# Kernel optimization log

Hardware: AMD Instinct MI355X
Metric: run time of the kernel (lower is better)

## Reference

```python
import jax, jax.numpy as jnp
import numpy as np

WINDOW_SIZE = 11
NUM_BINS = 256
SIGMA = 1.5
C1 = 0.01 ** 2
C2 = 0.03 ** 2
MAX_PSNR = 40.0


def _gaussian_window():
    xs = jnp.arange(WINDOW_SIZE, dtype=jnp.float32)
    g = jnp.exp(-((xs - WINDOW_SIZE // 2) ** 2) / (2.0 * SIGMA ** 2))
    g = g / g.sum()
    w2 = jnp.outer(g, g)  # [11,11]
    return jnp.broadcast_to(w2[None, None], (3, 1, WINDOW_SIZE, WINDOW_SIZE))


def setup_inputs() -> dict:
    key = jax.random.key(0)
    k1, k2 = jax.random.split(key)
    B, C, H, W = 64, 3, 256, 256
    x = jax.random.uniform(k1, (B, C, H, W), dtype=jnp.float32) * 2.0 - 1.0
    y = jax.random.uniform(k2, (B, C, H, W), dtype=jnp.float32) * 2.0 - 1.0
    return {"x": x, "y": y, "window": _gaussian_window()}


def _depthwise_conv(img, w):
    pad = WINDOW_SIZE // 2
    return jax.lax.conv_general_dilated(
        img, w, window_strides=(1, 1), padding=[(pad, pad), (pad, pad)],
        feature_group_count=img.shape[1],
        dimension_numbers=("NCHW", "OIHW", "NCHW"))


def _mi(x, y):
    B = x.shape[0]
    nb = NUM_BINS
    xf = (x.reshape(B, -1) + 1.0) * 0.5  # [B, N] in [0,1]
    yf = (y.reshape(B, -1) + 1.0) * 0.5
    N = xf.shape[1]
    ix = jnp.clip((xf * nb).astype(jnp.int32), 0, nb - 1)
    iy = jnp.clip((yf * nb).astype(jnp.int32), 0, nb - 1)
    flat = (jnp.arange(B, dtype=jnp.int32)[:, None] * (nb * nb) + ix * nb + iy).reshape(-1)
    hist = jnp.zeros(B * nb * nb, jnp.float32).at[flat].add(1.0).reshape(B, nb, nb)
    jp = hist / N  # joint probs [B, nb, nb]
    px = jp.sum(axis=2)  # [B, nb]
    py = jp.sum(axis=1)

    def ent(p):
        return -jnp.sum(jnp.where(p > 0, p * jnp.log2(jnp.where(p > 0, p, 1.0)), 0.0), axis=-1)

    hx = ent(px)
    hy = ent(py)
    pxy = px[:, :, None] * py[:, None, :]
    ratio = jp / jnp.where(pxy > 0, pxy, 1.0)
    mi = jnp.sum(jnp.where(jp > 0, jp * jnp.log2(jnp.where(jp > 0, ratio, 1.0)), 0.0), axis=(1, 2))
    norm = jnp.minimum(hx, hy)  # mi_method='min'
    mi = jnp.where(norm > 0, mi / norm, 0.0)
    return jnp.clip(mi, 0.0, 1.0)


def _ssim(x, y, window):
    mu1 = _depthwise_conv(x, window)
    mu2 = _depthwise_conv(y, window)
    mu1_sq = mu1 * mu1
    mu2_sq = mu2 * mu2
    mu1_mu2 = mu1 * mu2
    sigma1_sq = _depthwise_conv(x * x, window) - mu1_sq
    sigma2_sq = _depthwise_conv(y * y, window) - mu2_sq
    sigma12 = _depthwise_conv(x * y, window) - mu1_mu2
    ssim_map = ((2 * mu1_mu2 + C1) * (2 * sigma12 + C2)) / ((mu1_sq + mu2_sq + C1) * (sigma1_sq + sigma2_sq + C2))
    return ssim_map.mean(axis=(1, 2, 3))


def _psnr(x, y):
    xr = x * 0.5 + 0.5
    yr = y * 0.5 + 0.5
    mse = jnp.mean((xr - yr) ** 2, axis=(1, 2, 3))
    zero = mse == 0
    mse = jnp.where(zero, 1e-8, mse)
    psnr = -10.0 * jnp.log10(mse)  # 20*log10(1.0) == 0
    return jnp.where(zero, 100.0, psnr) / MAX_PSNR


def reference(x, y, window):
    mi_vals = _mi(x, y)
    ssim_vals = _ssim(x, y, window)
    psnr_vals = _psnr(x, y)
    metrics = jnp.stack([mi_vals, ssim_vals, psnr_vals], axis=1)  # [B,3]
    return metrics[:, :, None]  # [B,3,1]
```

## Files before the change

### kernel.cpp

```cpp
#include <hip/hip_runtime.h>
#include <cstdint>
#include <cstddef>

#define BATCH 64
#define CH 3
#define HH 256
#define WW 256
#define NBINS 256
#define TILE 32
#define HALO 5
#define NPB (CH*HH*WW)
#define QPX (NPB/4)

#define HISTA_SMEM (65536 + 64)
#define HISTB_SMEM (131072 + 4096 + 4096 + 1024 + 1024 + 64)

__device__ __forceinline__ float block_reduce_256(float v, float* buf4) {
    #pragma unroll
    for (int o = 32; o > 0; o >>= 1) v += __shfl_down(v, o, 64);
    __syncthreads();
    int lane = threadIdx.x & 63;
    int wid  = threadIdx.x >> 6;
    if (lane == 0) buf4[wid] = v;
    __syncthreads();
    return buf4[0] + buf4[1] + buf4[2] + buf4[3];
}

__device__ __forceinline__ float block_reduce_1024(float v, float* buf16) {
    #pragma unroll
    for (int o = 32; o > 0; o >>= 1) v += __shfl_down(v, o, 64);
    __syncthreads();
    int lane = threadIdx.x & 63;
    int wid  = threadIdx.x >> 6;
    if (lane == 0) buf16[wid] = v;
    __syncthreads();
    float s = 0.0f;
    #pragma unroll
    for (int i = 0; i < 16; i++) s += buf16[i];
    return s;
}

__global__ __launch_bounds__(256) void ssim_conv_kernel(
    const float* __restrict__ x, const float* __restrict__ y,
    const float* __restrict__ win,
    float* __restrict__ ssim_partials)
{
    __shared__ float hA[5][42][TILE];
    __shared__ float g[16];
    __shared__ float rbuf[4];

    const int tid = threadIdx.x;
    const int tx = blockIdx.x, ty = blockIdx.y, z = blockIdx.z;
    const float* xi = x + (size_t)z * (HH * WW);
    const float* yi = y + (size_t)z * (HH * WW);

    if (tid < 11) {
        float g5 = sqrtf(win[5*11 + 5]);
        g[tid] = win[5*11 + tid] / g5;
    }
    __syncthreads();

    for (int s = tid; s < 42 * 8; s += 256) {
        int r = s >> 3;
        int c0 = (s & 7) * 4;
        int gr = ty * TILE - HALO + r;
        int gw = tx * TILE + c0 - HALO;
        float xw[14], yw[14];
        bool rowok = (gr >= 0 && gr < HH);
        if (rowok) {
            const float* xr = xi + gr * WW;
            const float* yr = yi + gr * WW;
            int ga = gw - 3;
            if (ga >= 0 && ga + 20 <= WW) {
                float t0[20], t1[20];
                const float4* px4 = (const float4*)(xr + ga);
                const float4* py4 = (const float4*)(yr + ga);
                #pragma unroll
                for (int q = 0; q < 5; q++) {
                    float4 a = px4[q], b = py4[q];
                    t0[q*4+0]=a.x; t0[q*4+1]=a.y; t0[q*4+2]=a.z; t0[q*4+3]=a.w;
                    t1[q*4+0]=b.x; t1[q*4+1]=b.y; t1[q*4+2]=b.z; t1[q*4+3]=b.w;
                }
                #pragma unroll
                for (int i = 0; i < 14; i++) { xw[i] = t0[3+i]; yw[i] = t1[3+i]; }
            } else {
                #pragma unroll
                for (int i = 0; i < 14; i++) {
                    int gc = gw + i;
                    bool ok = (gc >= 0 && gc < WW);
                    xw[i] = ok ? xr[gc] : 0.0f;
                    yw[i] = ok ? yr[gc] : 0.0f;
                }
            }
        } else {
            #pragma unroll
            for (int i = 0; i < 14; i++) { xw[i] = 0.0f; yw[i] = 0.0f; }
        }

        float aX[4] = {0,0,0,0}, aY[4] = {0,0,0,0};
        float aXX[4] = {0,0,0,0}, aYY[4] = {0,0,0,0}, aXY[4] = {0,0,0,0};
        #pragma unroll
        for (int i = 0; i < 14; i++) {
            float xv = xw[i], yv = yw[i];
            float xx = xv * xv, yy = yv * yv, xy = xv * yv;
            #pragma unroll
            for (int j = 0; j < 4; j++) {
                int k = i - j;
                if (k >= 0 && k < 11) {
                    float w = g[k];
                    aX[j]  += w * xv;
                    aY[j]  += w * yv;
                    aXX[j] += w * xx;
                    aYY[j] += w * yy;
                    aXY[j] += w * xy;
                }
            }
        }
        *(float4*)&hA[0][r][c0] = make_float4(aX[0], aX[1], aX[2], aX[3]);
        *(float4*)&hA[1][r][c0] = make_float4(aY[0], aY[1], aY[2], aY[3]);
        *(float4*)&hA[2][r][c0] = make_float4(aXX[0], aXX[1], aXX[2], aXX[3]);
        *(float4*)&hA[3][r][c0] = make_float4(aYY[0], aYY[1], aYY[2], aYY[3]);
        *(float4*)&hA[4][r][c0] = make_float4(aXY[0], aXY[1], aXY[2], aXY[3]);
    }
    __syncthreads();

    const int c  = tid & 31;
    const int r0 = (tid >> 5) * 4;
    float mu1[4], mu2[4], exx[4], eyy[4], exy[4];
    #pragma unroll
    for (int j = 0; j < 4; j++) { mu1[j]=0; mu2[j]=0; exx[j]=0; eyy[j]=0; exy[j]=0; }
    #pragma unroll
    for (int a = 0; a < 5; a++) {
        float v[14];
        #pragma unroll
        for (int i = 0; i < 14; i++) v[i] = hA[a][r0 + i][c];
        #pragma unroll
        for (int k = 0; k < 11; k++) {
            float w = g[k];
            #pragma unroll
            for (int j = 0; j < 4; j++) {
                float t = w * v[j + k];
                if (a == 0) mu1[j] += t;
                else if (a == 1) mu2[j] += t;
                else if (a == 2) exx[j] += t;
                else if (a == 3) eyy[j] += t;
                else exy[j] += t;
            }
        }
    }

    float ssim_s = 0.0f;
    const float C1v = 1e-4f, C2v = 9e-4f;
    #pragma unroll
    for (int j = 0; j < 4; j++) {
        float m1 = mu1[j], m2 = mu2[j];
        float m1s = m1 * m1, m2s = m2 * m2, m12 = m1 * m2;
        float s1 = exx[j] - m1s, s2 = eyy[j] - m2s, s12 = exy[j] - m12;
        float num = (2.0f * m12 + C1v) * (2.0f * s12 + C2v);
        float den = (m1s + m2s + C1v) * (s1 + s2 + C2v);
        ssim_s += num / den;
    }

    float ssim_b = block_reduce_256(ssim_s, rbuf);
    if (tid == 0)
        ssim_partials[(size_t)z * 64 + ty * 8 + tx] = ssim_b;
}

__global__ __launch_bounds__(1024) void hist_mse_kernel(
    const float* __restrict__ x, const float* __restrict__ y,
    unsigned int* __restrict__ u8hist, float* __restrict__ mse_part)
{
    extern __shared__ char smem[];
    unsigned int* h32 = (unsigned int*)smem;
    float* rbuf = (float*)(smem + 65536);

    const int z = blockIdx.x, t = threadIdx.x;

    uint4* h128 = (uint4*)h32;
    #pragma unroll
    for (int i = 0; i < 4; i++) h128[t + i * 1024] = make_uint4(0, 0, 0, 0);
    __syncthreads();

    const float4* x4 = (const float4*)x + (size_t)(z >> 2) * (NPB/4) + (size_t)(z & 3) * (QPX/4);
    const float4* y4 = (const float4*)y + (size_t)(z >> 2) * (NPB/4) + (size_t)(z & 3) * (QPX/4);
    float mse_s = 0.0f;
    for (int i = 0; i < 12; i++) {
        float4 xv = x4[t + i * 1024];
        float4 yv = y4[t + i * 1024];
        float xs[4] = {xv.x, xv.y, xv.z, xv.w};
        float ys[4] = {yv.x, yv.y, yv.z, yv.w};
        #pragma unroll
        for (int e = 0; e < 4; e++) {
            float xc = xs[e], yc = ys[e];
            float d = xc - yc;
            mse_s += d * d;
            int ix = (int)(((xc + 1.0f) * 0.5f) * 256.0f);
            int iy = (int)(((yc + 1.0f) * 0.5f) * 256.0f);
            ix = min(max(ix, 0), 255);
            iy = min(max(iy, 0), 255);
            int key = ix * NBINS + iy;
            atomicAdd(&h32[key >> 2], 1u << (8 * (key & 3)));
        }
    }
    __syncthreads();

    float mse_total = block_reduce_1024(mse_s, rbuf);
    if (t == 0) mse_part[z] = mse_total;

    #pragma unroll
    for (int k = 0; k < 16; k++)
        u8hist[(size_t)z * 16384 + t + k * 1024] = h32[t + k * 1024];
}

__global__ __launch_bounds__(1024) void mi_final_kernel(
    const unsigned int* __restrict__ u8hist,
    const float* __restrict__ mse_part,
    const float* __restrict__ ssim_partials,
    float* __restrict__ out)
{
    extern __shared__ char smem[];
    unsigned int* h32 = (unsigned int*)smem;
    unsigned int* pxq = (unsigned int*)(smem + 131072);
    unsigned int* pyq = pxq + 1024;
    float* pxf = (float*)(pyq + 1024);
    float* pyf = pxf + 256;
    float* rbuf = pyf + 256;

    const int b = blockIdx.x, t = threadIdx.x;
    const float invN = 1.0f / (float)NPB;

    const uint4* p0 = (const uint4*)(u8hist + (size_t)(b * 4 + 0) * 16384);
    const uint4* p1 = (const uint4*)(u8hist + (size_t)(b * 4 + 1) * 16384);
    const uint4* p2 = (const uint4*)(u8hist + (size_t)(b * 4 + 2) * 16384);
    const uint4* p3 = (const uint4*)(u8hist + (size_t)(b * 4 + 3) * 16384);
    #pragma unroll
    for (int k4 = 0; k4 < 4; k4++) {
        int u = t + k4 * 1024;
        uint4 a = p0[u], c = p1[u], d = p2[u], e = p3[u];
        unsigned int wa[4] = {a.x, a.y, a.z, a.w};
        unsigned int wc[4] = {c.x, c.y, c.z, c.w};
        unsigned int wd[4] = {d.x, d.y, d.z, d.w};
        unsigned int we[4] = {e.x, e.y, e.z, e.w};
        unsigned int o[8];
        #pragma unroll
        for (int j = 0; j < 4; j++) {
            unsigned int lo = (wa[j] & 0x00FF00FFu) + (wc[j] & 0x00FF00FFu)
                            + (wd[j] & 0x00FF00FFu) + (we[j] & 0x00FF00FFu);
            unsigned int hi = ((wa[j] >> 8) & 0x00FF00FFu) + ((wc[j] >> 8) & 0x00FF00FFu)
                            + ((wd[j] >> 8) & 0x00FF00FFu) + ((we[j] >> 8) & 0x00FF00FFu);
            o[2*j]   = (lo & 0xFFFFu) | (hi << 16);
            o[2*j+1] = (lo >> 16) | (hi & 0xFFFF0000u);
        }
        *(uint4*)&h32[8 * (size_t)u]     = make_uint4(o[0], o[1], o[2], o[3]);
        *(uint4*)&h32[8 * (size_t)u + 4] = make_uint4(o[4], o[5], o[6], o[7]);
    }
    __syncthreads();

    {
        int r = t & 255, q = t >> 8;
        int base = r * 128 + q * 32;
        unsigned int s = 0;
        #pragma unroll
        for (int k = 0; k < 32; k++) {
            unsigned int v = h32[base + ((k + r) & 31)];
            s += (v & 0xFFFFu) + (v >> 16);
        }
        pxq[t] = s;
    }
    {
        int iy = t & 255, q = t >> 8;
        const unsigned short* h16 = (const unsigned short*)h32;
        unsigned int s = 0;
        #pragma unroll 8
        for (int ix = q * 64; ix < q * 64 + 64; ix++)
            s += h16[ix * NBINS + iy];
        pyq[t] = s;
    }
    __syncthreads();
    if (t < 256) {
        unsigned int pxc = pxq[t] + pxq[256 + t] + pxq[512 + t] + pxq[768 + t];
        unsigned int pyc = pyq[t] + pyq[256 + t] + pyq[512 + t] + pyq[768 + t];
        pxf[t] = (float)pxc * invN;
        pyf[t] = (float)pyc * invN;
    }
    __syncthreads();

    float ex = 0.0f, ey = 0.0f;
    if (t < 256) {
        float pv = pxf[t];
        if (pv > 0.0f) ex = -pv * __log2f(pv);
        pv = pyf[t];
        if (pv > 0.0f) ey = -pv * __log2f(pv);
    }
    float hx = block_reduce_1024(ex, rbuf);
    float hy = block_reduce_1024(ey, rbuf);

    float mi_s = 0.0f;
    {
        int iy = t & 255, q = t >> 8;
        const unsigned short* h16 = (const unsigned short*)h32;
        float pyv = pyf[iy];
        for (int ix = q * 64; ix < q * 64 + 64; ix++) {
            unsigned int hv = h16[ix * NBINS + iy];
            if (hv) {
                float jp = (float)hv * invN;
                mi_s += jp * log2f(jp / (pxf[ix] * pyv));
            }
        }
    }
    float mi = block_reduce_1024(mi_s, rbuf);
    float ssim_total = block_reduce_1024(
        (t < 192) ? ssim_partials[(size_t)b * 192 + t] : 0.0f, rbuf);

    if (t == 0) {
        float norm = fminf(hx, hy);
        float m = (norm > 0.0f) ? (mi / norm) : 0.0f;
        m = fminf(fmaxf(m, 0.0f), 1.0f);
        out[b * 3 + 0] = m;
        out[b * 3 + 1] = ssim_total * invN;
        float mse_total = mse_part[b * 4] + mse_part[b * 4 + 1]
                        + mse_part[b * 4 + 2] + mse_part[b * 4 + 3];
        double mse = (double)mse_total * (1.0 / (4.0 * (double)NPB));
        out[b * 3 + 2] = (mse == 0.0) ? 2.5f : (float)(-10.0 * log10(mse) / 40.0);
    }
}

extern "C" void kernel_launch(void* const* d_in, const int* in_sizes, int n_in,
                              void* d_out, int out_size, void* d_ws, size_t ws_size,
                              hipStream_t stream) {
    const float* x   = (const float*)d_in[0];
    const float* y   = (const float*)d_in[1];
    const float* win = (const float*)d_in[2];
    float* out = (float*)d_out;

    char* p = (char*)d_ws;
    unsigned int* u8hist = (unsigned int*)p;
    size_t off = (size_t)BATCH * 4 * 16384 * sizeof(unsigned int);
    float* mse_part = (float*)(p + off);       off += BATCH * 4 * sizeof(float);
    float* ssim_partials = (float*)(p + off);

    hipFuncSetAttribute((const void*)hist_mse_kernel,
                        hipFuncAttributeMaxDynamicSharedMemorySize, HISTA_SMEM);
    hipFuncSetAttribute((const void*)mi_final_kernel,
                        hipFuncAttributeMaxDynamicSharedMemorySize, HISTB_SMEM);

    dim3 grid(WW / TILE, HH / TILE, BATCH * CH);
    ssim_conv_kernel<<<grid, dim3(256), 0, stream>>>(x, y, win, ssim_partials);
    hist_mse_kernel<<<dim3(BATCH * 4), dim3(1024), HISTA_SMEM, stream>>>(
        x, y, u8hist, mse_part);
    mi_final_kernel<<<dim3(BATCH), dim3(1024), HISTB_SMEM, stream>>>(
        u8hist, mse_part, ssim_partials, out);
}
```

Baseline: 223.4 us.

## Compute MI via entropy identity and split histogram pass; taller SSIM tiles

The single 64-block MI kernel is replaced by a 256-block partial kernel. It merges the four sub-histograms in registers, accumulates joint entropy, row entropy and column counts through atomics, and feeds a small finalize kernel that uses MI = Hx + Hy - Hxy. This removes the 128KB shared-memory histogram build and the strided column scans, and spreads the work over more CUs. The SSIM tile also grows to 64 rows so each thread produces 8 outputs, which cuts halo overhead, at the cost of more registers. The change adds a memset and float atomics whose summation order is nondeterministic.

New measurement: 224.9 us. Within noise of the previous version (+0.7%).

```diff
diff --git a/kernel.cpp b/kernel.cpp
--- a/kernel.cpp
+++ b/kernel.cpp
@@ -7,13 +7,14 @@
 #define HH 256
 #define WW 256
 #define NBINS 256
-#define TILE 32
+#define TILE_W 32
+#define TILE_H 64
+#define HROWS (TILE_H + 10)
 #define HALO 5
 #define NPB (CH*HH*WW)
 #define QPX (NPB/4)
 
 #define HISTA_SMEM (65536 + 64)
-#define HISTB_SMEM (131072 + 4096 + 4096 + 1024 + 1024 + 64)
 
 __device__ __forceinline__ float block_reduce_256(float v, float* buf4) {
     #pragma unroll
@@ -45,7 +46,7 @@
     const float* __restrict__ win,
     float* __restrict__ ssim_partials)
 {
-    __shared__ float hA[5][42][TILE];
+    __shared__ float hA[5][HROWS][TILE_W];
     __shared__ float g[16];
     __shared__ float rbuf[4];
 
@@ -60,11 +61,11 @@
     }
     __syncthreads();
 
-    for (int s = tid; s < 42 * 8; s += 256) {
+    for (int s = tid; s < HROWS * 8; s += 256) {
         int r = s >> 3;
         int c0 = (s & 7) * 4;
-        int gr = ty * TILE - HALO + r;
-        int gw = tx * TILE + c0 - HALO;
+        int gr = ty * TILE_H - HALO + r;
+        int gw = tx * TILE_W + c0 - HALO;
         float xw[14], yw[14];
         bool rowok = (gr >= 0 && gr < HH);
         if (rowok) {
@@ -125,20 +126,20 @@
     __syncthreads();
 
     const int c  = tid & 31;
-    const int r0 = (tid >> 5) * 4;
-    float mu1[4], mu2[4], exx[4], eyy[4], exy[4];
-    #pragma unroll
-    for (int j = 0; j < 4; j++) { mu1[j]=0; mu2[j]=0; exx[j]=0; eyy[j]=0; exy[j]=0; }
+    const int r0 = (tid >> 5) * 8;
+    float mu1[8], mu2[8], exx[8], eyy[8], exy[8];
+    #pragma unroll
+    for (int j = 0; j < 8; j++) { mu1[j]=0; mu2[j]=0; exx[j]=0; eyy[j]=0; exy[j]=0; }
     #pragma unroll
     for (int a = 0; a < 5; a++) {
-        float v[14];
+        float v[18];
         #pragma unroll
-        for (int i = 0; i < 14; i++) v[i] = hA[a][r0 + i][c];
+        for (int i = 0; i < 18; i++) v[i] = hA[a][r0 + i][c];
         #pragma unroll
         for (int k = 0; k < 11; k++) {
             float w = g[k];
             #pragma unroll
-            for (int j = 0; j < 4; j++) {
+            for (int j = 0; j < 8; j++) {
                 float t = w * v[j + k];
                 if (a == 0) mu1[j] += t;
                 else if (a == 1) mu2[j] += t;
@@ -152,7 +153,7 @@
     float ssim_s = 0.0f;
     const float C1v = 1e-4f, C2v = 9e-4f;
     #pragma unroll
-    for (int j = 0; j < 4; j++) {
+    for (int j = 0; j < 8; j++) {
         float m1 = mu1[j], m2 = mu2[j];
         float m1s = m1 * m1, m2s = m2 * m2, m12 = m1 * m2;
         float s1 = exx[j] - m1s, s2 = eyy[j] - m2s, s12 = exy[j] - m12;
@@ -163,7 +164,7 @@
 
     float ssim_b = block_reduce_256(ssim_s, rbuf);
     if (tid == 0)
-        ssim_partials[(size_t)z * 64 + ty * 8 + tx] = ssim_b;
+        ssim_partials[(size_t)z * 32 + ty * 8 + tx] = ssim_b;
 }
 
 __global__ __launch_bounds__(1024) void hist_mse_kernel(
@@ -212,107 +213,97 @@
         u8hist[(size_t)z * 16384 + t + k * 1024] = h32[t + k * 1024];
 }
 
-__global__ __launch_bounds__(1024) void mi_final_kernel(
+__global__ __launch_bounds__(1024) void mi_partial_kernel(
     const unsigned int* __restrict__ u8hist,
-    const float* __restrict__ mse_part,
-    const float* __restrict__ ssim_partials,
+    float* __restrict__ hxy_acc, float* __restrict__ hx_acc,
+    unsigned int* __restrict__ py_acc)
+{
+    __shared__ unsigned int pyl[256];
+    __shared__ float rbuf[16];
+    const int b = blockIdx.x >> 2, s = blockIdx.x & 3, t = threadIdx.x;
+    const float invN = 1.0f / (float)NPB;
+
+    if (t < 256) pyl[t] = 0;
+    __syncthreads();
+
+    const uint4* base = (const uint4*)u8hist;
+    uint4 a = base[(size_t)(b * 4 + 0) * 4096 + s * 1024 + t];
+    uint4 c = base[(size_t)(b * 4 + 1) * 4096 + s * 1024 + t];
+    uint4 d = base[(size_t)(b * 4 + 2) * 4096 + s * 1024 + t];
+    uint4 e = base[(size_t)(b * 4 + 3) * 4096 + s * 1024 + t];
+    unsigned int wa[4] = {a.x, a.y, a.z, a.w};
+    unsigned int wc[4] = {c.x, c.y, c.z, c.w};
+    unsigned int wd[4] = {d.x, d.y, d.z, d.w};
+    unsigned int we[4] = {e.x, e.y, e.z, e.w};
+
+    unsigned int cnt[16];
+    #pragma unroll
+    for (int j = 0; j < 4; j++) {
+        unsigned int lo = (wa[j] & 0x00FF00FFu) + (wc[j] & 0x00FF00FFu)
+                        + (wd[j] & 0x00FF00FFu) + (we[j] & 0x00FF00FFu);
+        unsigned int hi = ((wa[j] >> 8) & 0x00FF00FFu) + ((wc[j] >> 8) & 0x00FF00FFu)
+                        + ((wd[j] >> 8) & 0x00FF00FFu) + ((we[j] >> 8) & 0x00FF00FFu);
+        cnt[4*j + 0] = lo & 0xFFFFu;
+        cnt[4*j + 1] = hi & 0xFFFFu;
+        cnt[4*j + 2] = lo >> 16;
+        cnt[4*j + 3] = hi >> 16;
+    }
+
+    float sxy = 0.0f;
+    unsigned int rowc = 0;
+    #pragma unroll
+    for (int k = 0; k < 16; k++) {
+        unsigned int v = cnt[k];
+        rowc += v;
+        if (v) {
+            float jp = (float)v * invN;
+            sxy += jp * __log2f(jp);
+        }
+        atomicAdd(&pyl[(16 * t + k) & 255], v);
+    }
+
+    #pragma unroll
+    for (int o = 8; o > 0; o >>= 1) rowc += __shfl_xor((int)rowc, o, 16);
+    float sx = 0.0f;
+    if ((t & 15) == 0 && rowc) {
+        float px = (float)rowc * invN;
+        sx = px * __log2f(px);
+    }
+
+    float sxy_blk = block_reduce_1024(sxy, rbuf);
+    float sx_blk  = block_reduce_1024(sx, rbuf);
+    __syncthreads();
+    if (t < 256) atomicAdd(&py_acc[b * 256 + t], pyl[t]);
+    if (t == 0) {
+        atomicAdd(&hxy_acc[b], sxy_blk);
+        atomicAdd(&hx_acc[b],  sx_blk);
+    }
+}
+
+__global__ __launch_bounds__(256) void finalize_kernel(
+    const unsigned int* __restrict__ py_acc,
+    const float* __restrict__ hxy_acc, const float* __restrict__ hx_acc,
+    const float* __restrict__ mse_part, const float* __restrict__ ssim_partials,
     float* __restrict__ out)
 {
-    extern __shared__ char smem[];
-    unsigned int* h32 = (unsigned int*)smem;
-    unsigned int* pxq = (unsigned int*)(smem + 131072);
-    unsigned int* pyq = pxq + 1024;
-    float* pxf = (float*)(pyq + 1024);
-    float* pyf = pxf + 256;
-    float* rbuf = pyf + 256;
-
+    __shared__ float rbuf[4];
     const int b = blockIdx.x, t = threadIdx.x;
     const float invN = 1.0f / (float)NPB;
 
-    const uint4* p0 = (const uint4*)(u8hist + (size_t)(b * 4 + 0) * 16384);
-    const uint4* p1 = (const uint4*)(u8hist + (size_t)(b * 4 + 1) * 16384);
-    const uint4* p2 = (const uint4*)(u8hist + (size_t)(b * 4 + 2) * 16384);
-    const uint4* p3 = (const uint4*)(u8hist + (size_t)(b * 4 + 3) * 16384);
-    #pragma unroll
-    for (int k4 = 0; k4 < 4; k4++) {
-        int u = t + k4 * 1024;
-        uint4 a = p0[u], c = p1[u], d = p2[u], e = p3[u];
-        unsigned int wa[4] = {a.x, a.y, a.z, a.w};
-        unsigned int wc[4] = {c.x, c.y, c.z, c.w};
-        unsigned int wd[4] = {d.x, d.y, d.z, d.w};
-        unsigned int we[4] = {e.x, e.y, e.z, e.w};
-        unsigned int o[8];
-        #pragma unroll
-        for (int j = 0; j < 4; j++) {
-            unsigned int lo = (wa[j] & 0x00FF00FFu) + (wc[j] & 0x00FF00FFu)
-                            + (wd[j] & 0x00FF00FFu) + (we[j] & 0x00FF00FFu);
-            unsigned int hi = ((wa[j] >> 8) & 0x00FF00FFu) + ((wc[j] >> 8) & 0x00FF00FFu)
-                            + ((wd[j] >> 8) & 0x00FF00FFu) + ((we[j] >> 8) & 0x00FF00FFu);
-            o[2*j]   = (lo & 0xFFFFu) | (hi << 16);
-            o[2*j+1] = (lo >> 16) | (hi & 0xFFFF0000u);
-        }
-        *(uint4*)&h32[8 * (size_t)u]     = make_uint4(o[0], o[1], o[2], o[3]);
-        *(uint4*)&h32[8 * (size_t)u + 4] = make_uint4(o[4], o[5], o[6], o[7]);
-    }
-    __syncthreads();
-
-    {
-        int r = t & 255, q = t >> 8;
-        int base = r * 128 + q * 32;
-        unsigned int s = 0;
-        #pragma unroll
-        for (int k = 0; k < 32; k++) {
-            unsigned int v = h32[base + ((k + r) & 31)];
-            s += (v & 0xFFFFu) + (v >> 16);
-        }
-        pxq[t] = s;
-    }
-    {
-        int iy = t & 255, q = t >> 8;
-        const unsigned short* h16 = (const unsigned short*)h32;
-        unsigned int s = 0;
-        #pragma unroll 8
-        for (int ix = q * 64; ix < q * 64 + 64; ix++)
-            s += h16[ix * NBINS + iy];
-        pyq[t] = s;
-    }
-    __syncthreads();
-    if (t < 256) {
-        unsigned int pxc = pxq[t] + pxq[256 + t] + pxq[512 + t] + pxq[768 + t];
-        unsigned int pyc = pyq[t] + pyq[256 + t] + pyq[512 + t] + pyq[768 + t];
-        pxf[t] = (float)pxc * invN;
-        pyf[t] = (float)pyc * invN;
-    }
-    __syncthreads();
-
-    float ex = 0.0f, ey = 0.0f;
-    if (t < 256) {
-        float pv = pxf[t];
-        if (pv > 0.0f) ex = -pv * __log2f(pv);
-        pv = pyf[t];
-        if (pv > 0.0f) ey = -pv * __log2f(pv);
-    }
-    float hx = block_reduce_1024(ex, rbuf);
-    float hy = block_reduce_1024(ey, rbuf);
-
-    float mi_s = 0.0f;
-    {
-        int iy = t & 255, q = t >> 8;
-        const unsigned short* h16 = (const unsigned short*)h32;
-        float pyv = pyf[iy];
-        for (int ix = q * 64; ix < q * 64 + 64; ix++) {
-            unsigned int hv = h16[ix * NBINS + iy];
-            if (hv) {
-                float jp = (float)hv * invN;
-                mi_s += jp * log2f(jp / (pxf[ix] * pyv));
-            }
-        }
-    }
-    float mi = block_reduce_1024(mi_s, rbuf);
-    float ssim_total = block_reduce_1024(
-        (t < 192) ? ssim_partials[(size_t)b * 192 + t] : 0.0f, rbuf);
+    float ey = 0.0f;
+    unsigned int pyc = py_acc[b * 256 + t];
+    if (pyc) {
+        float py = (float)pyc * invN;
+        ey = -py * __log2f(py);
+    }
+    float hy = block_reduce_256(ey, rbuf);
+    float ssim_total = block_reduce_256(
+        (t < 96) ? ssim_partials[(size_t)b * 96 + t] : 0.0f, rbuf);
 
     if (t == 0) {
+        float hx  = -hx_acc[b];
+        float hxy = -hxy_acc[b];
+        float mi = hx + hy - hxy;
         float norm = fminf(hx, hy);
         float m = (norm > 0.0f) ? (mi / norm) : 0.0f;
         m = fminf(fmaxf(m, 0.0f), 1.0f);
@@ -334,20 +325,26 @@
     float* out = (float*)d_out;
 
     char* p = (char*)d_ws;
-    unsigned int* u8hist = (unsigned int*)p;
-    size_t off = (size_t)BATCH * 4 * 16384 * sizeof(unsigned int);
+    unsigned int* py_acc = (unsigned int*)p;
+    float* hxy_acc = (float*)(p + 65536);
+    float* hx_acc  = (float*)(p + 65536 + 256);
+    size_t zero_bytes = 65536 + 512;
+    unsigned int* u8hist = (unsigned int*)(p + zero_bytes);
+    size_t off = zero_bytes + (size_t)BATCH * 4 * 16384 * sizeof(unsigned int);
     float* mse_part = (float*)(p + off);       off += BATCH * 4 * sizeof(float);
     float* ssim_partials = (float*)(p + off);
 
+    hipMemsetAsync(p, 0, zero_bytes, stream);
+
     hipFuncSetAttribute((const void*)hist_mse_kernel,
                         hipFuncAttributeMaxDynamicSharedMemorySize, HISTA_SMEM);
-    hipFuncSetAttribute((const void*)mi_final_kernel,
-                        hipFuncAttributeMaxDynamicSharedMemorySize, HISTB_SMEM);
-
-    dim3 grid(WW / TILE, HH / TILE, BATCH * CH);
+
+    dim3 grid(WW / TILE_W, HH / TILE_H, BATCH * CH);
     ssim_conv_kernel<<<grid, dim3(256), 0, stream>>>(x, y, win, ssim_partials);
     hist_mse_kernel<<<dim3(BATCH * 4), dim3(1024), HISTA_SMEM, stream>>>(
         x, y, u8hist, mse_part);
-    mi_final_kernel<<<dim3(BATCH), dim3(1024), HISTB_SMEM, stream>>>(
-        u8hist, mse_part, ssim_partials, out);
-}
+    mi_partial_kernel<<<dim3(BATCH * 4), dim3(1024), 0, stream>>>(
+        u8hist, hxy_acc, hx_acc, py_acc);
+    finalize_kernel<<<dim3(BATCH), dim3(256), 0, stream>>>(
+        py_acc, hxy_acc, hx_acc, mse_part, ssim_partials, out);
+}
```
